# Kernel optimization log

Hardware: AMD Instinct MI355X
Metric: run time of the kernel (lower is better)

The kernel has to match this reference:

```python
import jax, jax.numpy as jnp
import numpy as np

B, S, D, H = 4, 1024, 1024, 16
HD = D // H


def setup_inputs() -> dict:
    key = jax.random.key(0)
    ks = jax.random.split(key, 8)
    x = jax.random.normal(ks[0], (B, S, D), dtype=jnp.float32)
    attn_bias = jax.random.normal(ks[1], (B, H, S, S), dtype=jnp.float32) * 0.1
    pos_ids = jnp.broadcast_to(jnp.arange(S, dtype=jnp.int32), (B, S))
    lengths = jnp.array([S, S - 64, S - 128, S - 256], dtype=jnp.int32)
    pad_mask = jnp.arange(S)[None, :] >= lengths[:, None]  # True = padded key
    scale = 0.02
    Wq = jax.random.normal(ks[2], (D, D), dtype=jnp.float32) * scale
    Wk = jax.random.normal(ks[3], (D, D), dtype=jnp.float32) * scale
    Wv = jax.random.normal(ks[4], (D, D), dtype=jnp.float32) * scale
    Wo = jax.random.normal(ks[5], (D, D), dtype=jnp.float32) * scale
    bq = jnp.zeros((D,), jnp.float32); bk = jnp.zeros((D,), jnp.float32)
    bv = jnp.zeros((D,), jnp.float32); bo = jnp.zeros((D,), jnp.float32)
    return {"x": x, "attn_bias": attn_bias, "pos_ids": pos_ids, "pad_mask": pad_mask,
            "Wq": Wq, "bq": bq, "Wk": Wk, "bk": bk, "Wv": Wv, "bv": bv, "Wo": Wo, "bo": bo}


def _apply_rotary(q, k, pos_ids):
    # q,k: [B,S,H,HD]; pos_ids: [B,S]
    hd = q.shape[-1]
    inv_freq = 1.0 / (10000.0 ** (jnp.arange(0, hd, 2, dtype=jnp.float32) / hd))
    freqs = pos_ids.astype(jnp.float32)[:, :, None] * inv_freq  # [B,S,HD/2]
    emb = jnp.concatenate([freqs, freqs], axis=-1)[:, :, None, :]  # [B,S,1,HD]
    cos, sin = jnp.cos(emb), jnp.sin(emb)
    def rot_half(t):
        t1, t2 = jnp.split(t, 2, axis=-1)
        return jnp.concatenate([-t2, t1], axis=-1)
    return q * cos + rot_half(q) * sin, k * cos + rot_half(k) * sin


def reference(x, attn_bias, pos_ids, pad_mask, Wq, bq, Wk, bk, Wv, bv, Wo, bo):
    b, s, d = x.shape
    q = (x @ Wq.T + bq).reshape(b, s, H, HD)
    k = (x @ Wk.T + bk).reshape(b, s, H, HD)
    v = (x @ Wv.T + bv).reshape(b, s, H, HD)
    q, k = _apply_rotary(q, k, pos_ids)
    q = q.transpose(0, 2, 1, 3)  # [B,H,S,HD]
    k = k.transpose(0, 2, 1, 3)
    v = v.transpose(0, 2, 1, 3)
    scores = jnp.einsum("bhqd,bhkd->bhqk", q, k) / np.sqrt(HD).astype(np.float32)
    scores = scores + attn_bias
    scores = jnp.where(pad_mask[:, None, None, :], -jnp.inf, scores)
    attn = jax.nn.softmax(scores, axis=-1)  # dropout p=0 -> identity
    out = jnp.einsum("bhqk,bhkd->bqhd", attn, v).reshape(b, s, d)
    metric = k.mean(axis=1)  # mean over heads -> [B,S,HD]
    return out @ Wo.T + bo, metric
```

## Files before the change

### kernel.cpp

```cpp
#include <hip/hip_runtime.h>
#include <hip/hip_bf16.h>

#define SS 1024
#define DD 1024
#define HH 16
#define HDD 64

using f32x4  = __attribute__((ext_vector_type(4))) float;
using bf16x8 = __attribute__((ext_vector_type(8))) __bf16;
using bf16x4 = __attribute__((ext_vector_type(4))) __bf16;

__device__ __forceinline__ void gload_lds16(const void* g, void* l) {
  __builtin_amdgcn_global_load_lds((__attribute__((address_space(1))) void*)g,
                                   (__attribute__((address_space(3))) void*)l, 16, 0, 0);
}

__global__ void convert_kernel(const float4* __restrict__ x, const float4* __restrict__ Wq,
                               const float4* __restrict__ Wk, const float4* __restrict__ Wv,
                               const float4* __restrict__ Wo,
                               bf16x4* __restrict__ xb, bf16x4* __restrict__ wqkvb,
                               bf16x4* __restrict__ wob) {
  int i = blockIdx.x * 256 + threadIdx.x;
  float4 v; bf16x4* dst;
  if (i < 1048576)      { v = x[i];              dst = xb + i; }
  else if (i < 1310720) { v = Wq[i - 1048576];   dst = wqkvb + (i - 1048576); }
  else if (i < 1572864) { v = Wk[i - 1310720];   dst = wqkvb + 262144 + (i - 1310720); }
  else if (i < 1835008) { v = Wv[i - 1572864];   dst = wqkvb + 524288 + (i - 1572864); }
  else                  { v = Wo[i - 1835008];   dst = wob + (i - 1835008); }
  bf16x4 o;
  o[0] = (__bf16)v.x; o[1] = (__bf16)v.y; o[2] = (__bf16)v.z; o[3] = (__bf16)v.w;
  *dst = o;
}

__global__ void prep_kernel(const __bf16* __restrict__ wqkv, const float* __restrict__ bk,
                            __bf16* __restrict__ wkavg, float* __restrict__ bkavg) {
  int idx = blockIdx.x * 512 + threadIdx.x;
  int d = idx >> 7, k8 = (idx & 127) * 8;
  float s[8] = {};
#pragma unroll
  for (int h = 0; h < 16; ++h) {
    bf16x8 v = *(const bf16x8*)(wqkv + (size_t)(1024 + h * 64 + d) * 1024 + k8);
#pragma unroll
    for (int j = 0; j < 8; ++j) s[j] += (float)v[j];
  }
  bf16x8 o;
#pragma unroll
  for (int j = 0; j < 8; ++j) o[j] = (__bf16)(s[j] * 0.0625f);
  *(bf16x8*)(wkavg + (size_t)d * 1024 + k8) = o;
  if (blockIdx.x == 0 && threadIdx.x < 64) {
    float b = 0.f;
#pragma unroll
    for (int h = 0; h < 16; ++h) b += bk[h * 64 + threadIdx.x];
    bkavg[threadIdx.x] = b * 0.0625f;
  }
}

#define GEMM_STAGE(BUF, KK)                                                        \
  {                                                                                \
    char* Ab = smem + (BUF) * 32768;                                               \
    char* Bb = Ab + 16384;                                                         \
    _Pragma("unroll") for (int q = 0; q < 4; ++q) {                                \
      int idx = q * 256 + tid;                                                     \
      int row = idx >> 3, c = idx & 7;                                             \
      gload_lds16(A  + (size_t)(m0 + row) * 1024 + (KK) + ((c ^ (row & 7)) << 3),  \
                  Ab + q * 4096 + wid * 1024);                                     \
      gload_lds16(Bm + (size_t)(n0 + row) * 1024 + (KK) + ((c ^ (row & 7)) << 3),  \
                  Bb + q * 4096 + wid * 1024);                                     \
    }                                                                              \
  }

template<int EPI>
__global__ __launch_bounds__(256, 2)
void gemm_kernel(const __bf16* __restrict__ A, const __bf16* __restrict__ Bm, int N,
                 const float* __restrict__ b0, const float* __restrict__ b1,
                 const float* __restrict__ b2, const float* __restrict__ bavg,
                 const int* __restrict__ pos_ids,
                 __bf16* __restrict__ Qr, __bf16* __restrict__ Kr, __bf16* __restrict__ Vtg,
                 float* __restrict__ metric, float* __restrict__ Cout) {
  __shared__ __align__(16) char smem[65536];
  const int tid = threadIdx.x;
  const int wid = tid >> 6, lane = tid & 63;
  const int g = lane >> 4, cl = lane & 15;
  const int ntn = N >> 7;
  const int tile = (blockIdx.x & 7) * ((int)gridDim.x >> 3) + (blockIdx.x >> 3);
  const int bm = tile / ntn, bn = tile % ntn;
  const int m0 = bm << 7, n0 = bn << 7;
  const int wr = (wid >> 1) << 6, wc = (wid & 1) << 6;
  const int swz = cl & 7;

  f32x4 acc[4][4] = {};

  GEMM_STAGE(0, 0);
  __syncthreads();
  int buf = 0;
  for (int t = 0; t < 16; ++t) {
    if (t + 1 < 16) GEMM_STAGE(buf ^ 1, (t + 1) * 64);
    const __bf16* Abuf = (const __bf16*)(smem + buf * 32768);
    const __bf16* Bbuf = Abuf + 8192;
#pragma unroll
    for (int s = 0; s < 2; ++s) {
      bf16x8 fa[4], fb[4];
#pragma unroll
      for (int i = 0; i < 4; ++i)
        fa[i] = *(const bf16x8*)(Abuf + (wr + i * 16 + cl) * 64 + (((s * 4 + g) ^ swz) << 3));
#pragma unroll
      for (int j = 0; j < 4; ++j)
        fb[j] = *(const bf16x8*)(Bbuf + (wc + j * 16 + cl) * 64 + (((s * 4 + g) ^ swz) << 3));
#pragma unroll
      for (int i = 0; i < 4; ++i)
#pragma unroll
        for (int j = 0; j < 4; ++j)
          acc[i][j] = __builtin_amdgcn_mfma_f32_16x16x32_bf16(fa[i], fb[j], acc[i][j], 0, 0, 0);
    }
    __syncthreads();
    buf ^= 1;
  }

  if constexpr (EPI == 1) {
#pragma unroll
    for (int j = 0; j < 4; ++j) {
      int col = n0 + wc + j * 16 + cl;
      float bv = b0[col];
#pragma unroll
      for (int i = 0; i < 4; ++i)
#pragma unroll
        for (int r = 0; r < 4; ++r) {
          int row = m0 + wr + i * 16 + g * 4 + r;
          Cout[(size_t)row * 1024 + col] = acc[i][j][r] + bv;
        }
    }
  } else if (n0 >= 3072) {
    if (wc == 0) {
      float invf0 = exp2f(-0.4152410118609203f * (float)(cl));
      float invf1 = exp2f(-0.4152410118609203f * (float)(16 + cl));
#pragma unroll
      for (int i = 0; i < 4; ++i) {
#pragma unroll
        for (int r = 0; r < 4; ++r) {
          int row = m0 + wr + i * 16 + g * 4 + r;
          float pos = (float)pos_ids[row];
#pragma unroll
          for (int j = 0; j < 2; ++j) {
            int dlo = j * 16 + cl;
            float vlo = acc[i][j][r]     + bavg[dlo];
            float vhi = acc[i][j + 2][r] + bavg[dlo + 32];
            float th = pos * (j == 0 ? invf0 : invf1);
            float sn, cs;
            __sincosf(th, &sn, &cs);
            metric[(size_t)row * HDD + dlo]      = vlo * cs - vhi * sn;
            metric[(size_t)row * HDD + dlo + 32] = vhi * cs + vlo * sn;
          }
        }
      }
    }
  } else if (n0 >= 2048) {
    __bf16* vt_s = (__bf16*)smem;
    const int b_ = m0 >> 10, s0 = m0 & 1023;
    const int vbase = n0 - 2048;
#pragma unroll
    for (int phase = 0; phase < 2; ++phase) {
      __syncthreads();
      if ((wid & 1) == phase) {
#pragma unroll
        for (int j = 0; j < 4; ++j) {
          int d = j * 16 + cl;
          float bv = b2[vbase + wc + d];
#pragma unroll
          for (int i = 0; i < 4; ++i)
#pragma unroll
            for (int r = 0; r < 4; ++r)
              vt_s[d * 136 + wr + i * 16 + g * 4 + r] = (__bf16)(acc[i][j][r] + bv);
        }
      }
      __syncthreads();
      int hh = (vbase >> 6) + phase;
#pragma unroll
      for (int p = 0; p < 4; ++p) {
        int d = p * 16 + (tid >> 4), s8 = (tid & 15) * 8;
        bf16x8 v = *(const bf16x8*)(vt_s + d * 136 + s8);
        *(bf16x8*)(Vtg + ((size_t)(b_ * HH + hh) * HDD + d) * SS + s0 + s8) = v;
      }
    }
  } else {
    const int cb = n0 + wc;
    const int region = cb >> 10;
    const int hcol = (cb & 1023) >> 6;
    const int cir = cb & 1023;
    const float* bias = region == 0 ? b0 : b1;
    __bf16* dst = region == 0 ? Qr : Kr;
    float invf0 = exp2f(-0.4152410118609203f * (float)(cl));
    float invf1 = exp2f(-0.4152410118609203f * (float)(16 + cl));
#pragma unroll
    for (int i = 0; i < 4; ++i) {
#pragma unroll
      for (int r = 0; r < 4; ++r) {
        int row = m0 + wr + i * 16 + g * 4 + r;
        int b_ = row >> 10, s = row & 1023;
        size_t ob = ((size_t)(b_ * HH + hcol) * SS + s) * HDD;
        float pos = (float)pos_ids[row];
#pragma unroll
        for (int j = 0; j < 2; ++j) {
          int dlo = j * 16 + cl;
          float vlo = acc[i][j][r]     + bias[cir + dlo];
          float vhi = acc[i][j + 2][r] + bias[cir + dlo + 32];
          float th = pos * (j == 0 ? invf0 : invf1);
          float sn, cs;
          __sincosf(th, &sn, &cs);
          float olo = vlo * cs - vhi * sn;
          float ohi = vhi * cs + vlo * sn;
          dst[ob + dlo]      = (__bf16)olo;
          dst[ob + dlo + 32] = (__bf16)ohi;
        }
      }
    }
  }
}

#define ATTN_HALF(KT0, W0, BCUR)                                                   \
  {                                                                                \
    f32x4 sc[4];                                                                   \
    __builtin_amdgcn_s_setprio(1);                                                 \
    _Pragma("unroll") for (int kt = 0; kt < 4; ++kt) {                             \
      int row = (KT0 + kt) * 16 + cl;                                              \
      bf16x8 kb0 = *(const bf16x8*)(&Ks[buf][row][(g ^ swz) * 8]);                 \
      bf16x8 kb1 = *(const bf16x8*)(&Ks[buf][row][((g + 4) ^ swz) * 8]);           \
      f32x4 z = {0.f, 0.f, 0.f, 0.f};                                              \
      z = __builtin_amdgcn_mfma_f32_16x16x32_bf16(kb0, aq0, z, 0, 0, 0);           \
      sc[kt] = __builtin_amdgcn_mfma_f32_16x16x32_bf16(kb1, aq1, z, 0, 0, 0);      \
    }                                                                              \
    __builtin_amdgcn_s_setprio(0);                                                 \
    _Pragma("unroll") for (int kt = 0; kt < 4; ++kt)                               \
      _Pragma("unroll") for (int r = 0; r < 4; ++r)                                \
        sc[kt][r] = sc[kt][r] * 0.125f + BCUR[KT0 + kt][r];                        \
    float mx = fmaxf(fmaxf(fmaxf(sc[0][0], sc[0][1]), fmaxf(sc[0][2], sc[0][3])),  \
                     fmaxf(fmaxf(sc[1][0], sc[1][1]), fmaxf(sc[1][2], sc[1][3]))); \
    mx = fmaxf(mx, fmaxf(fmaxf(fmaxf(sc[2][0], sc[2][1]), fmaxf(sc[2][2], sc[2][3])), \
                         fmaxf(fmaxf(sc[3][0], sc[3][1]), fmaxf(sc[3][2], sc[3][3])))); \
    mx = fmaxf(mx, __shfl_xor(mx, 16, 64));                                        \
    mx = fmaxf(mx, __shfl_xor(mx, 32, 64));                                        \
    if (!__all(mx <= m_l + 8.0f)) {                                                \
      float nm = fmaxf(m_l, mx);                                                   \
      float s_ = __expf(m_l - nm);                                                 \
      m_l = nm; l_l *= s_;                                                         \
      float sb0 = __shfl(s_, 4 * g + 0, 64), sb1 = __shfl(s_, 4 * g + 1, 64);      \
      float sb2 = __shfl(s_, 4 * g + 2, 64), sb3 = __shfl(s_, 4 * g + 3, 64);      \
      _Pragma("unroll") for (int dj = 0; dj < 4; ++dj) {                           \
        o[dj][0] *= sb0; o[dj][1] *= sb1; o[dj][2] *= sb2; o[dj][3] *= sb3;        \
      }                                                                            \
    }                                                                              \
    _Pragma("unroll") for (int kt = 0; kt < 4; ++kt)                               \
      _Pragma("unroll") for (int r = 0; r < 4; ++r)                                \
        sc[kt][r] = __expf(sc[kt][r] - m_l);                                       \
    float rs = ((sc[0][0] + sc[0][1]) + (sc[0][2] + sc[0][3]))                     \
             + ((sc[1][0] + sc[1][1]) + (sc[1][2] + sc[1][3]))                     \
             + ((sc[2][0] + sc[2][1]) + (sc[2][2] + sc[2][3]))                     \
             + ((sc[3][0] + sc[3][1]) + (sc[3][2] + sc[3][3]));                    \
    rs += __shfl_xor(rs, 16, 64);                                                  \
    rs += __shfl_xor(rs, 32, 64);                                                  \
    l_l += rs;                                                                     \
    _Pragma("unroll") for (int w = 0; w < 2; ++w) {                                \
      _Pragma("unroll") for (int k2 = 0; k2 < 2; ++k2) {                           \
        int kt = w * 2 + k2;                                                       \
        bf16x4 pk;                                                                 \
        pk[0] = (__bf16)sc[kt][0]; pk[1] = (__bf16)sc[kt][1];                      \
        pk[2] = (__bf16)sc[kt][2]; pk[3] = (__bf16)sc[kt][3];                      \
        *(bf16x4*)(Pw + cl * 40 + k2 * 16 + 4 * g) = pk;                           \
      }                                                                            \
      bf16x8 pa = *(const bf16x8*)(Pw + cl * 40 + g * 8);                          \
      __builtin_amdgcn_s_setprio(1);                                               \
      _Pragma("unroll") for (int dj = 0; dj < 4; ++dj) {                           \
        int vrow = dj * 16 + cl;                                                   \
        bf16x8 vb = *(const bf16x8*)(&Vt[buf][vrow][((((W0 + w) * 4) + g) ^ swz) * 8]); \
        o[dj] = __builtin_amdgcn_mfma_f32_16x16x32_bf16(pa, vb, o[dj], 0, 0, 0);   \
      }                                                                            \
      __builtin_amdgcn_s_setprio(0);                                               \
    }                                                                              \
  }

#define ATTN_STAGE(NB, KK)                                                         \
  _Pragma("unroll") for (int s = 0; s < 2; ++s) {                                  \
    gload_lds16(Kb + (size_t)((KK) + s * 64 + krow) * 64 + kchk * 8,               \
                (char*)&Ks[NB][s * 64 + 8 * wid][0]);                              \
    gload_lds16(Vb + (size_t)(s * 32 + vrow) * SS + (KK) + vchk * 8,               \
                (char*)&Vt[NB][s * 32 + 4 * wid][0]);                              \
  }

__global__ __launch_bounds__(512, 4)
void attn_kernel(const __bf16* __restrict__ Qr, const __bf16* __restrict__ Kr,
                 const __bf16* __restrict__ Vtg, const float* __restrict__ bias,
                 const int* __restrict__ pad, __bf16* __restrict__ attn_out) {
  __shared__ __align__(16) __bf16 Ks[2][128][64];
  __shared__ __align__(16) __bf16 Vt[2][64][128];
  __shared__ __align__(16) __bf16 Plds[8][16][40];
  const int tid = threadIdx.x;
  const int wid = tid >> 6, lane = tid & 63;
  const int g = lane >> 4, cl = lane & 15;
  const int bh = blockIdx.x & 63, b_ = bh >> 4, h = bh & 15;
  const int q0 = (blockIdx.x >> 6) * 128 + wid * 16;
  const __bf16* Qb = Qr  + ((size_t)bh << 16);
  const __bf16* Kb = Kr  + ((size_t)bh << 16);
  const __bf16* Vb = Vtg + ((size_t)bh << 16);
  const float*  Bb = bias + ((size_t)bh << 20);
  const int* padb = pad + b_ * SS;

  int pm = (lane < 16) ? padb[lane * 64] : 1;
  unsigned long long ball = __ballot(pm == 0);
  const int valid64 = __popcll(ball & 0xFFFFull);
  const int nt = (valid64 + 1) >> 1;
  const int tail = valid64 & 1;

  const int krow = 8 * wid + (lane >> 3);
  const int kchk = (lane & 7) ^ (lane >> 3);
  const int vrow = 4 * wid + (lane >> 4);
  const int vchk = (lane & 15) ^ (vrow & 7);
  const int swz = cl & 7;
  __bf16* Pw = &Plds[wid][0][0];

  bf16x8 aq0 = *(const bf16x8*)(Qb + (size_t)(q0 + cl) * 64 + g * 8);
  bf16x8 aq1 = *(const bf16x8*)(Qb + (size_t)(q0 + cl) * 64 + 32 + g * 8);
  __builtin_amdgcn_sched_barrier(0);

  ATTN_STAGE(0, 0);
  __builtin_amdgcn_sched_barrier(0);
  f32x4 breg[8];
#pragma unroll
  for (int kt = 0; kt < 8; ++kt)
    breg[kt] = *(const f32x4*)(Bb + (size_t)(q0 + cl) * SS + kt * 16 + 4 * g);
  __builtin_amdgcn_sched_barrier(0);

  f32x4 o[4] = {};
  float m_l = -1e30f, l_l = 0.f;

  for (int t = 0; t < nt; ++t) {
    const int buf = t & 1;
    asm volatile("s_waitcnt vmcnt(8)" ::: "memory");
    __builtin_amdgcn_s_barrier();
    __builtin_amdgcn_sched_barrier(0);
    if (t + 1 < nt) {
      ATTN_STAGE(buf ^ 1, (t + 1) * 128);
      __builtin_amdgcn_sched_barrier(0);
    }

    ATTN_HALF(0, 0, breg);

    if (t + 1 < nt) {
      int kk2 = (t + 1) * 128;
#pragma unroll
      for (int kt = 0; kt < 4; ++kt)
        breg[kt] = *(const f32x4*)(Bb + (size_t)(q0 + cl) * SS + kk2 + kt * 16 + 4 * g);
      __builtin_amdgcn_sched_barrier(0);
    }

    if (!(tail && t == nt - 1))
      ATTN_HALF(4, 2, breg);

    if (t + 1 < nt) {
      int kk2 = (t + 1) * 128;
#pragma unroll
      for (int kt = 4; kt < 8; ++kt)
        breg[kt] = *(const f32x4*)(Bb + (size_t)(q0 + cl) * SS + kk2 + kt * 16 + 4 * g);
      __builtin_amdgcn_sched_barrier(0);
    }
  }

  float lb0 = __shfl(l_l, 4 * g + 0, 64), lb1 = __shfl(l_l, 4 * g + 1, 64);
  float lb2 = __shfl(l_l, 4 * g + 2, 64), lb3 = __shfl(l_l, 4 * g + 3, 64);
  float ib0 = 1.f / lb0, ib1 = 1.f / lb1, ib2 = 1.f / lb2, ib3 = 1.f / lb3;
#pragma unroll
  for (int dj = 0; dj < 4; ++dj) {
    int col = h * 64 + dj * 16 + cl;
    attn_out[(size_t)(b_ * SS + q0 + g * 4 + 0) * DD + col] = (__bf16)(o[dj][0] * ib0);
    attn_out[(size_t)(b_ * SS + q0 + g * 4 + 1) * DD + col] = (__bf16)(o[dj][1] * ib1);
    attn_out[(size_t)(b_ * SS + q0 + g * 4 + 2) * DD + col] = (__bf16)(o[dj][2] * ib2);
    attn_out[(size_t)(b_ * SS + q0 + g * 4 + 3) * DD + col] = (__bf16)(o[dj][3] * ib3);
  }
}

extern "C" void kernel_launch(void* const* d_in, const int* in_sizes, int n_in,
                              void* d_out, int out_size, void* d_ws, size_t ws_size,
                              hipStream_t stream) {
  const float* x  = (const float*)d_in[0];
  const float* ab = (const float*)d_in[1];
  const int* pos  = (const int*)d_in[2];
  const int* pad  = (const int*)d_in[3];
  const float* Wq = (const float*)d_in[4];
  const float* bq = (const float*)d_in[5];
  const float* Wk = (const float*)d_in[6];
  const float* bk = (const float*)d_in[7];
  const float* Wv = (const float*)d_in[8];
  const float* bv = (const float*)d_in[9];
  const float* Wo = (const float*)d_in[10];
  const float* bo = (const float*)d_in[11];
  float* out = (float*)d_out;
  float* metric = out + 4194304;

  char* ws = (char*)d_ws;
  __bf16* Qr    = (__bf16*)(ws);
  __bf16* Kr    = (__bf16*)(ws + 8388608);
  __bf16* Vtg   = (__bf16*)(ws + 16777216);
  __bf16* xb    = (__bf16*)(ws + 25165824);
  __bf16* wqkv  = (__bf16*)(ws + 33554432);
  __bf16* wob   = (__bf16*)(ws + 40108032);
  __bf16* ao    = (__bf16*)(ws + 42205184);
  float*  bkavg = (float*)(ws + 50593792);

  convert_kernel<<<8192, 256, 0, stream>>>((const float4*)x, (const float4*)Wq,
                                           (const float4*)Wk, (const float4*)Wv,
                                           (const float4*)Wo, (bf16x4*)xb,
                                           (bf16x4*)wqkv, (bf16x4*)wob);
  prep_kernel<<<16, 512, 0, stream>>>(wqkv, bk, wqkv + (size_t)3072 * 1024, bkavg);
  gemm_kernel<0><<<800, 256, 0, stream>>>(xb, wqkv, 3200, bq, bk, bv, bkavg, pos,
                                          Qr, Kr, Vtg, metric, nullptr);
  attn_kernel<<<512, 512, 0, stream>>>(Qr, Kr, Vtg, ab, pad, ao);
  gemm_kernel<1><<<256, 256, 0, stream>>>(ao, wob, 1024, bo, nullptr, nullptr, nullptr,
                                          nullptr, nullptr, nullptr, nullptr, nullptr, out);
}
```

Before: 143.7 us.

## Read attention K/V directly from global and retile output projection to 128x64

The attention kernel drops its LDS double-buffered K/V staging, barriers and bias prefetch pipeline. It now loads K and V fragments straight from global memory (relying on L1/L2), with 256-thread blocks over 64 queries and twice as many blocks. The output-projection GEMM becomes a dedicated kernel with 128x64 tiles, doubling its grid to 512 blocks for better CU occupancy. The trade-off is more global/cache traffic and less latency hiding in attention, since the prefetch and software pipelining are removed.

```diff
diff --git a/kernel.cpp b/kernel.cpp
--- a/kernel.cpp
+++ b/kernel.cpp
@@ -69,14 +69,13 @@
     }                                                                              \
   }
 
-template<int EPI>
 __global__ __launch_bounds__(256, 2)
-void gemm_kernel(const __bf16* __restrict__ A, const __bf16* __restrict__ Bm, int N,
-                 const float* __restrict__ b0, const float* __restrict__ b1,
-                 const float* __restrict__ b2, const float* __restrict__ bavg,
-                 const int* __restrict__ pos_ids,
-                 __bf16* __restrict__ Qr, __bf16* __restrict__ Kr, __bf16* __restrict__ Vtg,
-                 float* __restrict__ metric, float* __restrict__ Cout) {
+void gemm_qkv(const __bf16* __restrict__ A, const __bf16* __restrict__ Bm, int N,
+              const float* __restrict__ b0, const float* __restrict__ b1,
+              const float* __restrict__ b2, const float* __restrict__ bavg,
+              const int* __restrict__ pos_ids,
+              __bf16* __restrict__ Qr, __bf16* __restrict__ Kr, __bf16* __restrict__ Vtg,
+              float* __restrict__ metric) {
   __shared__ __align__(16) char smem[65536];
   const int tid = threadIdx.x;
   const int wid = tid >> 6, lane = tid & 63;
@@ -116,20 +115,7 @@
     buf ^= 1;
   }
 
-  if constexpr (EPI == 1) {
-#pragma unroll
-    for (int j = 0; j < 4; ++j) {
-      int col = n0 + wc + j * 16 + cl;
-      float bv = b0[col];
-#pragma unroll
-      for (int i = 0; i < 4; ++i)
-#pragma unroll
-        for (int r = 0; r < 4; ++r) {
-          int row = m0 + wr + i * 16 + g * 4 + r;
-          Cout[(size_t)row * 1024 + col] = acc[i][j][r] + bv;
-        }
-    }
-  } else if (n0 >= 3072) {
+  if (n0 >= 3072) {
     if (wc == 0) {
       float invf0 = exp2f(-0.4152410118609203f * (float)(cl));
       float invf1 = exp2f(-0.4152410118609203f * (float)(16 + cl));
@@ -216,14 +202,87 @@
   }
 }
 
-#define ATTN_HALF(KT0, W0, BCUR)                                                   \
+__global__ __launch_bounds__(256, 2)
+void gemm_oproj(const __bf16* __restrict__ A, const __bf16* __restrict__ Bm,
+                const float* __restrict__ b0, float* __restrict__ Cout) {
+  __shared__ __align__(16) char smem[49152];
+  const int tid = threadIdx.x;
+  const int wid = tid >> 6, lane = tid & 63;
+  const int g = lane >> 4, cl = lane & 15;
+  const int tile = (blockIdx.x & 7) * 64 + (blockIdx.x >> 3);
+  const int bm = tile >> 4, bn = tile & 15;
+  const int m0 = bm << 7, n0 = bn << 6;
+  const int wr = (wid >> 1) << 6, wc = (wid & 1) << 5;
+  const int swz = cl & 7;
+
+  f32x4 acc[4][2] = {};
+
+#define OP_STAGE(BUF, KK)                                                          \
+  {                                                                                \
+    char* Ab = smem + (BUF) * 24576;                                               \
+    char* Bb2 = Ab + 16384;                                                        \
+    _Pragma("unroll") for (int q = 0; q < 4; ++q) {                                \
+      int idx = q * 256 + tid;                                                     \
+      int row = idx >> 3, c = idx & 7;                                             \
+      gload_lds16(A + (size_t)(m0 + row) * 1024 + (KK) + ((c ^ (row & 7)) << 3),   \
+                  Ab + q * 4096 + wid * 1024);                                     \
+    }                                                                              \
+    _Pragma("unroll") for (int q = 0; q < 2; ++q) {                                \
+      int idx = q * 256 + tid;                                                     \
+      int row = idx >> 3, c = idx & 7;                                             \
+      gload_lds16(Bm + (size_t)(n0 + row) * 1024 + (KK) + ((c ^ (row & 7)) << 3),  \
+                  Bb2 + q * 4096 + wid * 1024);                                    \
+    }                                                                              \
+  }
+
+  OP_STAGE(0, 0);
+  __syncthreads();
+  int buf = 0;
+  for (int t = 0; t < 16; ++t) {
+    if (t + 1 < 16) OP_STAGE(buf ^ 1, (t + 1) * 64);
+    const __bf16* Abuf = (const __bf16*)(smem + buf * 24576);
+    const __bf16* Bbuf = (const __bf16*)(smem + buf * 24576 + 16384);
+#pragma unroll
+    for (int s = 0; s < 2; ++s) {
+      bf16x8 fa[4], fb[2];
+#pragma unroll
+      for (int i = 0; i < 4; ++i)
+        fa[i] = *(const bf16x8*)(Abuf + (wr + i * 16 + cl) * 64 + (((s * 4 + g) ^ swz) << 3));
+#pragma unroll
+      for (int j = 0; j < 2; ++j)
+        fb[j] = *(const bf16x8*)(Bbuf + (wc + j * 16 + cl) * 64 + (((s * 4 + g) ^ swz) << 3));
+#pragma unroll
+      for (int i = 0; i < 4; ++i)
+#pragma unroll
+        for (int j = 0; j < 2; ++j)
+          acc[i][j] = __builtin_amdgcn_mfma_f32_16x16x32_bf16(fa[i], fb[j], acc[i][j], 0, 0, 0);
+    }
+    __syncthreads();
+    buf ^= 1;
+  }
+
+#pragma unroll
+  for (int j = 0; j < 2; ++j) {
+    int col = n0 + wc + j * 16 + cl;
+    float bv = b0[col];
+#pragma unroll
+    for (int i = 0; i < 4; ++i)
+#pragma unroll
+      for (int r = 0; r < 4; ++r) {
+        int row = m0 + wr + i * 16 + g * 4 + r;
+        Cout[(size_t)row * 1024 + col] = acc[i][j][r] + bv;
+      }
+  }
+}
+
+#define ATTN_HALF_D(KOFF, BI)                                                      \
   {                                                                                \
     f32x4 sc[4];                                                                   \
     __builtin_amdgcn_s_setprio(1);                                                 \
     _Pragma("unroll") for (int kt = 0; kt < 4; ++kt) {                             \
-      int row = (KT0 + kt) * 16 + cl;                                              \
-      bf16x8 kb0 = *(const bf16x8*)(&Ks[buf][row][(g ^ swz) * 8]);                 \
-      bf16x8 kb1 = *(const bf16x8*)(&Ks[buf][row][((g + 4) ^ swz) * 8]);           \
+      const __bf16* kp = Kb + (size_t)(kk + (KOFF) + kt * 16 + cl) * 64;           \
+      bf16x8 kb0 = *(const bf16x8*)(kp + g * 8);                                   \
+      bf16x8 kb1 = *(const bf16x8*)(kp + 32 + g * 8);                              \
       f32x4 z = {0.f, 0.f, 0.f, 0.f};                                              \
       z = __builtin_amdgcn_mfma_f32_16x16x32_bf16(kb0, aq0, z, 0, 0, 0);           \
       sc[kt] = __builtin_amdgcn_mfma_f32_16x16x32_bf16(kb1, aq1, z, 0, 0, 0);      \
@@ -231,7 +290,7 @@
     __builtin_amdgcn_s_setprio(0);                                                 \
     _Pragma("unroll") for (int kt = 0; kt < 4; ++kt)                               \
       _Pragma("unroll") for (int r = 0; r < 4; ++r)                                \
-        sc[kt][r] = sc[kt][r] * 0.125f + BCUR[KT0 + kt][r];                        \
+        sc[kt][r] = sc[kt][r] * 0.125f + breg[(BI) + kt][r];                       \
     float mx = fmaxf(fmaxf(fmaxf(sc[0][0], sc[0][1]), fmaxf(sc[0][2], sc[0][3])),  \
                      fmaxf(fmaxf(sc[1][0], sc[1][1]), fmaxf(sc[1][2], sc[1][3]))); \
     mx = fmaxf(mx, fmaxf(fmaxf(fmaxf(sc[2][0], sc[2][1]), fmaxf(sc[2][2], sc[2][3])), \
@@ -269,34 +328,23 @@
       bf16x8 pa = *(const bf16x8*)(Pw + cl * 40 + g * 8);                          \
       __builtin_amdgcn_s_setprio(1);                                               \
       _Pragma("unroll") for (int dj = 0; dj < 4; ++dj) {                           \
-        int vrow = dj * 16 + cl;                                                   \
-        bf16x8 vb = *(const bf16x8*)(&Vt[buf][vrow][((((W0 + w) * 4) + g) ^ swz) * 8]); \
+        bf16x8 vb = *(const bf16x8*)(Vb + (size_t)(dj * 16 + cl) * SS + kk + (KOFF) + w * 32 + g * 8); \
         o[dj] = __builtin_amdgcn_mfma_f32_16x16x32_bf16(pa, vb, o[dj], 0, 0, 0);   \
       }                                                                            \
       __builtin_amdgcn_s_setprio(0);                                               \
     }                                                                              \
   }
 
-#define ATTN_STAGE(NB, KK)                                                         \
-  _Pragma("unroll") for (int s = 0; s < 2; ++s) {                                  \
-    gload_lds16(Kb + (size_t)((KK) + s * 64 + krow) * 64 + kchk * 8,               \
-                (char*)&Ks[NB][s * 64 + 8 * wid][0]);                              \
-    gload_lds16(Vb + (size_t)(s * 32 + vrow) * SS + (KK) + vchk * 8,               \
-                (char*)&Vt[NB][s * 32 + 4 * wid][0]);                              \
-  }
-
-__global__ __launch_bounds__(512, 4)
+__global__ __launch_bounds__(256, 4)
 void attn_kernel(const __bf16* __restrict__ Qr, const __bf16* __restrict__ Kr,
                  const __bf16* __restrict__ Vtg, const float* __restrict__ bias,
                  const int* __restrict__ pad, __bf16* __restrict__ attn_out) {
-  __shared__ __align__(16) __bf16 Ks[2][128][64];
-  __shared__ __align__(16) __bf16 Vt[2][64][128];
-  __shared__ __align__(16) __bf16 Plds[8][16][40];
+  __shared__ __align__(16) __bf16 Plds[4][16][40];
   const int tid = threadIdx.x;
   const int wid = tid >> 6, lane = tid & 63;
   const int g = lane >> 4, cl = lane & 15;
   const int bh = blockIdx.x & 63, b_ = bh >> 4, h = bh & 15;
-  const int q0 = (blockIdx.x >> 6) * 128 + wid * 16;
+  const int q0 = (blockIdx.x >> 6) * 64 + wid * 16;
   const __bf16* Qb = Qr  + ((size_t)bh << 16);
   const __bf16* Kb = Kr  + ((size_t)bh << 16);
   const __bf16* Vb = Vtg + ((size_t)bh << 16);
@@ -309,58 +357,24 @@
   const int nt = (valid64 + 1) >> 1;
   const int tail = valid64 & 1;
 
-  const int krow = 8 * wid + (lane >> 3);
-  const int kchk = (lane & 7) ^ (lane >> 3);
-  const int vrow = 4 * wid + (lane >> 4);
-  const int vchk = (lane & 15) ^ (vrow & 7);
-  const int swz = cl & 7;
   __bf16* Pw = &Plds[wid][0][0];
 
   bf16x8 aq0 = *(const bf16x8*)(Qb + (size_t)(q0 + cl) * 64 + g * 8);
   bf16x8 aq1 = *(const bf16x8*)(Qb + (size_t)(q0 + cl) * 64 + 32 + g * 8);
-  __builtin_amdgcn_sched_barrier(0);
-
-  ATTN_STAGE(0, 0);
-  __builtin_amdgcn_sched_barrier(0);
-  f32x4 breg[8];
-#pragma unroll
-  for (int kt = 0; kt < 8; ++kt)
-    breg[kt] = *(const f32x4*)(Bb + (size_t)(q0 + cl) * SS + kt * 16 + 4 * g);
-  __builtin_amdgcn_sched_barrier(0);
 
   f32x4 o[4] = {};
   float m_l = -1e30f, l_l = 0.f;
 
   for (int t = 0; t < nt; ++t) {
-    const int buf = t & 1;
-    asm volatile("s_waitcnt vmcnt(8)" ::: "memory");
-    __builtin_amdgcn_s_barrier();
-    __builtin_amdgcn_sched_barrier(0);
-    if (t + 1 < nt) {
-      ATTN_STAGE(buf ^ 1, (t + 1) * 128);
-      __builtin_amdgcn_sched_barrier(0);
-    }
-
-    ATTN_HALF(0, 0, breg);
-
-    if (t + 1 < nt) {
-      int kk2 = (t + 1) * 128;
-#pragma unroll
-      for (int kt = 0; kt < 4; ++kt)
-        breg[kt] = *(const f32x4*)(Bb + (size_t)(q0 + cl) * SS + kk2 + kt * 16 + 4 * g);
-      __builtin_amdgcn_sched_barrier(0);
-    }
-
+    const int kk = t * 128;
+    f32x4 breg[8];
+#pragma unroll
+    for (int kt = 0; kt < 8; ++kt)
+      breg[kt] = *(const f32x4*)(Bb + (size_t)(q0 + cl) * SS + kk + kt * 16 + 4 * g);
+
+    ATTN_HALF_D(0, 0);
     if (!(tail && t == nt - 1))
-      ATTN_HALF(4, 2, breg);
-
-    if (t + 1 < nt) {
-      int kk2 = (t + 1) * 128;
-#pragma unroll
-      for (int kt = 4; kt < 8; ++kt)
-        breg[kt] = *(const f32x4*)(Bb + (size_t)(q0 + cl) * SS + kk2 + kt * 16 + 4 * g);
-      __builtin_amdgcn_sched_barrier(0);
-    }
+      ATTN_HALF_D(64, 4);
   }
 
   float lb0 = __shfl(l_l, 4 * g + 0, 64), lb1 = __shfl(l_l, 4 * g + 1, 64);
@@ -409,9 +423,8 @@
                                            (const float4*)Wo, (bf16x4*)xb,
                                            (bf16x4*)wqkv, (bf16x4*)wob);
   prep_kernel<<<16, 512, 0, stream>>>(wqkv, bk, wqkv + (size_t)3072 * 1024, bkavg);
-  gemm_kernel<0><<<800, 256, 0, stream>>>(xb, wqkv, 3200, bq, bk, bv, bkavg, pos,
-                                          Qr, Kr, Vtg, metric, nullptr);
-  attn_kernel<<<512, 512, 0, stream>>>(Qr, Kr, Vtg, ab, pad, ao);
-  gemm_kernel<1><<<256, 256, 0, stream>>>(ao, wob, 1024, bo, nullptr, nullptr, nullptr,
-                                          nullptr, nullptr, nullptr, nullptr, nullptr, out);
-}
+  gemm_qkv<<<800, 256, 0, stream>>>(xb, wqkv, 3200, bq, bk, bv, bkavg, pos,
+                                    Qr, Kr, Vtg, metric);
+  attn_kernel<<<1024, 256, 0, stream>>>(Qr, Kr, Vtg, ab, pad, ao);
+  gemm_oproj<<<512, 256, 0, stream>>>(ao, wob, bo, out);
+}
```

New measurement: 227.5 us. 1.58x slower.
